# Optimization experiments

Hardware: AMD Instinct MI355X
Metric: run time of the kernel (lower is better)

## Reference

```python
import jax, jax.numpy as jnp
import numpy as np

EPS = 1e-08
MAX_DELTA_LOG = 0.3
N = 1_000_000
DEG = 4
E = N * DEG
H = 64


def setup_inputs() -> dict:
    key = jax.random.key(0)
    k1, k2, k3, k4, k5, k6 = jax.random.split(key, 6)
    hu_scalar = jax.random.normal(k1, (N,), dtype=jnp.float32) * 50.0 + 100.0
    neighbor_indices = jax.random.randint(k2, (E,), 0, N, dtype=jnp.int64)
    neighbor_offsets = (jnp.arange(N + 1, dtype=jnp.int64) * DEG)  # fixed degree-4 CSR
    W_nei1 = jax.random.normal(k3, (1, H), dtype=jnp.float32) * 0.01
    W_self1 = jax.random.normal(k4, (1, H), dtype=jnp.float32) * 0.01
    b1 = jnp.zeros((H,), dtype=jnp.float32)
    W_nei2 = jax.random.normal(k5, (H,), dtype=jnp.float32) * 0.01
    W_self2 = jax.random.normal(k6, (H,), dtype=jnp.float32) * 0.01
    b2 = jnp.zeros((1,), dtype=jnp.float32)
    return {
        'hu_scalar': hu_scalar,
        'neighbor_indices': neighbor_indices,
        'neighbor_offsets': neighbor_offsets,
        'W_nei1': W_nei1,
        'W_self1': W_self1,
        'b1': b1,
        'W_nei2': W_nei2,
        'W_self2': W_self2,
        'b2': b2,
    }


def reference(hu_scalar, neighbor_indices, neighbor_offsets, W_nei1, W_self1, b1, W_nei2, W_self2, b2):
    n = neighbor_offsets.shape[0] - 1
    e = neighbor_indices.shape[0]
    counts = neighbor_offsets[1:] - neighbor_offsets[:-1]
    # CSR row ids for each edge: repeat_interleave(arange(N), counts)
    row_ids = jnp.repeat(jnp.arange(n, dtype=jnp.int64), counts, total_repeat_length=e)

    h = hu_scalar.astype(jnp.float32)
    mu = h.mean()
    sigma = h.std(ddof=1) + EPS  # torch.std is unbiased
    h0 = (h - mu) / sigma  # (N,)

    # layer 1: scatter-sum of scalar neighbor features
    nei_sum0 = jax.ops.segment_sum(h0[neighbor_indices], row_ids, num_segments=n)  # (N,)
    h1 = jax.nn.relu(b1 + nei_sum0[:, None] * W_nei1 + h0[:, None] * W_self1)  # (N, H)

    # layer 2: scatter-sum of (N,H) features
    nei_sum1 = jax.ops.segment_sum(h1[neighbor_indices], row_ids, num_segments=n)  # (N, H)
    delta_raw = b2 + nei_sum1 @ W_nei2 + h1 @ W_self2  # (N,)
    return MAX_DELTA_LOG * jnp.tanh(delta_raw)
```

## Files before the change

kernel.cpp:

```cpp
#include <hip/hip_runtime.h>
#include <math.h>

#define RED_BLOCKS 1024
#define BLK 256
#define HDIM 64

__global__ void k_reduce_partial(const float* __restrict__ hu, int n,
                                 double* __restrict__ part) {
  __shared__ double ls[BLK];
  __shared__ double lq[BLK];
  double s = 0.0, q = 0.0;
  for (int i = blockIdx.x * BLK + threadIdx.x; i < n; i += gridDim.x * BLK) {
    double v = (double)hu[i];
    s += v;
    q += v * v;
  }
  ls[threadIdx.x] = s;
  lq[threadIdx.x] = q;
  __syncthreads();
  for (int off = BLK / 2; off > 0; off >>= 1) {
    if (threadIdx.x < off) {
      ls[threadIdx.x] += ls[threadIdx.x + off];
      lq[threadIdx.x] += lq[threadIdx.x + off];
    }
    __syncthreads();
  }
  if (threadIdx.x == 0) {
    part[blockIdx.x] = ls[0];
    part[RED_BLOCKS + blockIdx.x] = lq[0];
  }
}

__global__ void k_reduce_final(const double* __restrict__ part, int n,
                               float* __restrict__ stats) {
  __shared__ double ls[BLK];
  __shared__ double lq[BLK];
  double s = 0.0, q = 0.0;
  for (int i = threadIdx.x; i < RED_BLOCKS; i += BLK) {
    s += part[i];
    q += part[RED_BLOCKS + i];
  }
  ls[threadIdx.x] = s;
  lq[threadIdx.x] = q;
  __syncthreads();
  for (int off = BLK / 2; off > 0; off >>= 1) {
    if (threadIdx.x < off) {
      ls[threadIdx.x] += ls[threadIdx.x + off];
      lq[threadIdx.x] += lq[threadIdx.x + off];
    }
    __syncthreads();
  }
  if (threadIdx.x == 0) {
    double sum = ls[0], sumsq = lq[0];
    double mu = sum / (double)n;
    double var = (sumsq - sum * sum / (double)n) / (double)(n - 1);
    if (var < 0.0) var = 0.0;
    double sigma = sqrt(var) + 1e-8;
    stats[0] = (float)mu;
    stats[1] = (float)(1.0 / sigma);
  }
}

__global__ void k_layer1(const float* __restrict__ hu,
                         const int* __restrict__ nbr,
                         const float* __restrict__ Wn1,
                         const float* __restrict__ Ws1,
                         const float* __restrict__ B1,
                         const float* __restrict__ Wn2,
                         const float* __restrict__ Ws2,
                         const float* __restrict__ stats,
                         float* __restrict__ snei,
                         float* __restrict__ sself,
                         int n) {
  __shared__ float wn1[HDIM], ws1[HDIM], bb1[HDIM], wn2[HDIM], ws2[HDIM];
  int t = threadIdx.x;
  if (t < HDIM) {
    wn1[t] = Wn1[t];
    ws1[t] = Ws1[t];
    bb1[t] = B1[t];
    wn2[t] = Wn2[t];
    ws2[t] = Ws2[t];
  }
  __syncthreads();
  int u = blockIdx.x * BLK + threadIdx.x;
  if (u >= n) return;
  float mu = stats[0];
  float inv = stats[1];
  int4 nb = ((const int4*)nbr)[u];
  float hsum = hu[nb.x] + hu[nb.y] + hu[nb.z] + hu[nb.w];
  float a = (hsum - 4.0f * mu) * inv;
  float c = (hu[u] - mu) * inv;
  float sn = 0.0f, ss = 0.0f;
#pragma unroll
  for (int j = 0; j < HDIM; ++j) {
    float tt = fmaf(a, wn1[j], fmaf(c, ws1[j], bb1[j]));
    float r = fmaxf(tt, 0.0f);
    sn = fmaf(r, wn2[j], sn);
    ss = fmaf(r, ws2[j], ss);
  }
  snei[u] = sn;
  if (sself != nullptr) sself[u] = ss;
}

__global__ void k_layer2(const int* __restrict__ nbr,
                         const float* __restrict__ snei,
                         const float* __restrict__ sself,
                         const float* __restrict__ B2,
                         float* __restrict__ out,
                         int n) {
  int u = blockIdx.x * BLK + threadIdx.x;
  if (u >= n) return;
  int4 nb = ((const int4*)nbr)[u];
  float s = snei[nb.x] + snei[nb.y] + snei[nb.z] + snei[nb.w];
  float d = B2[0] + s + sself[u];
  out[u] = 0.3f * tanhf(d);
}

__global__ void k_layer2_rc(const float* __restrict__ hu,
                            const int* __restrict__ nbr,
                            const float* __restrict__ Wn1,
                            const float* __restrict__ Ws1,
                            const float* __restrict__ B1,
                            const float* __restrict__ Ws2,
                            const float* __restrict__ stats,
                            const float* __restrict__ snei,
                            const float* __restrict__ B2,
                            float* __restrict__ out,
                            int n) {
  __shared__ float wn1[HDIM], ws1[HDIM], bb1[HDIM], ws2[HDIM];
  int t = threadIdx.x;
  if (t < HDIM) {
    wn1[t] = Wn1[t];
    ws1[t] = Ws1[t];
    bb1[t] = B1[t];
    ws2[t] = Ws2[t];
  }
  __syncthreads();
  int u = blockIdx.x * BLK + threadIdx.x;
  if (u >= n) return;
  float mu = stats[0];
  float inv = stats[1];
  int4 nb = ((const int4*)nbr)[u];
  float hsum = hu[nb.x] + hu[nb.y] + hu[nb.z] + hu[nb.w];
  float a = (hsum - 4.0f * mu) * inv;
  float c = (hu[u] - mu) * inv;
  float ss = 0.0f;
#pragma unroll
  for (int j = 0; j < HDIM; ++j) {
    float tt = fmaf(a, wn1[j], fmaf(c, ws1[j], bb1[j]));
    float r = fmaxf(tt, 0.0f);
    ss = fmaf(r, ws2[j], ss);
  }
  float s = snei[nb.x] + snei[nb.y] + snei[nb.z] + snei[nb.w];
  float d = B2[0] + s + ss;
  out[u] = 0.3f * tanhf(d);
}

extern "C" void kernel_launch(void* const* d_in, const int* in_sizes, int n_in,
                              void* d_out, int out_size, void* d_ws, size_t ws_size,
                              hipStream_t stream) {
  const float* hu  = (const float*)d_in[0];
  const int*   nbr = (const int*)d_in[1];
  const float* Wn1 = (const float*)d_in[3];
  const float* Ws1 = (const float*)d_in[4];
  const float* B1  = (const float*)d_in[5];
  const float* Wn2 = (const float*)d_in[6];
  const float* Ws2 = (const float*)d_in[7];
  const float* B2  = (const float*)d_in[8];
  float* out = (float*)d_out;
  const int n = in_sizes[0];

  char* ws = (char*)d_ws;
  double* part = (double*)ws;
  float* stats = (float*)(ws + 2 * RED_BLOCKS * 8);
  float* snei  = (float*)(ws + 32768);
  size_t need_full = 32768 + 2 * (size_t)n * sizeof(float);
  size_t need_half = 32768 + (size_t)n * sizeof(float);

  k_reduce_partial<<<RED_BLOCKS, BLK, 0, stream>>>(hu, n, part);
  k_reduce_final<<<1, BLK, 0, stream>>>(part, n, stats);

  int blocks = (n + BLK - 1) / BLK;
  if (ws_size >= need_full) {
    float* sself = snei + n;
    k_layer1<<<blocks, BLK, 0, stream>>>(hu, nbr, Wn1, Ws1, B1, Wn2, Ws2, stats,
                                         snei, sself, n);
    k_layer2<<<blocks, BLK, 0, stream>>>(nbr, snei, sself, B2, out, n);
  } else if (ws_size >= need_half) {
    k_layer1<<<blocks, BLK, 0, stream>>>(hu, nbr, Wn1, Ws1, B1, Wn2, Ws2, stats,
                                         snei, nullptr, n);
    k_layer2_rc<<<blocks, BLK, 0, stream>>>(hu, nbr, Wn1, Ws1, B1, Ws2, stats,
                                            snei, B2, out, n);
  }
}
```

Baseline: 63.55 us.

## Vectorize reduction and layer-1 loop, use nontemporal loads/stores, drop fallback path

The stats reduction now reads hu as float4 and handles the tail on one thread. Layer-1's hidden loop works on 4-wide float vectors held in shared memory, and the neighbor index loads and the intermediate and output stores become nontemporal. Launch bounds are added everywhere, and the recompute fallback for a small workspace is removed, so a full-size workspace is now assumed. The aim is fewer memory instructions and less cache pollution from streamed data, at the cost of failing if the workspace is smaller than 2N floats.

```diff
diff --git a/kernel.cpp b/kernel.cpp
--- a/kernel.cpp
+++ b/kernel.cpp
@@ -5,15 +5,28 @@
 #define BLK 256
 #define HDIM 64
 
-__global__ void k_reduce_partial(const float* __restrict__ hu, int n,
-                                 double* __restrict__ part) {
+typedef int   v4i __attribute__((ext_vector_type(4)));
+typedef float v4f __attribute__((ext_vector_type(4)));
+
+__global__ void __launch_bounds__(BLK) k_reduce_partial(const float* __restrict__ hu, int n,
+                                                        double* __restrict__ part) {
   __shared__ double ls[BLK];
   __shared__ double lq[BLK];
+  const v4f* hu4 = (const v4f*)hu;
+  const int n4 = n >> 2;
   double s = 0.0, q = 0.0;
-  for (int i = blockIdx.x * BLK + threadIdx.x; i < n; i += gridDim.x * BLK) {
-    double v = (double)hu[i];
-    s += v;
-    q += v * v;
+  for (int i = blockIdx.x * BLK + threadIdx.x; i < n4; i += RED_BLOCKS * BLK) {
+    v4f v = hu4[i];
+    double a = (double)v.x, b = (double)v.y, c = (double)v.z, d = (double)v.w;
+    s += a + b + c + d;
+    q += a * a + b * b + c * c + d * d;
+  }
+  if (blockIdx.x == 0 && threadIdx.x == 0) {
+    for (int i = n4 << 2; i < n; ++i) {
+      double v = (double)hu[i];
+      s += v;
+      q += v * v;
+    }
   }
   ls[threadIdx.x] = s;
   lq[threadIdx.x] = q;
@@ -31,8 +44,8 @@
   }
 }
 
-__global__ void k_reduce_final(const double* __restrict__ part, int n,
-                               float* __restrict__ stats) {
+__global__ void __launch_bounds__(BLK) k_reduce_final(const double* __restrict__ part, int n,
+                                                      float* __restrict__ stats) {
   __shared__ double ls[BLK];
   __shared__ double lq[BLK];
   double s = 0.0, q = 0.0;
@@ -61,99 +74,67 @@
   }
 }
 
-__global__ void k_layer1(const float* __restrict__ hu,
-                         const int* __restrict__ nbr,
-                         const float* __restrict__ Wn1,
-                         const float* __restrict__ Ws1,
-                         const float* __restrict__ B1,
-                         const float* __restrict__ Wn2,
-                         const float* __restrict__ Ws2,
-                         const float* __restrict__ stats,
-                         float* __restrict__ snei,
-                         float* __restrict__ sself,
-                         int n) {
-  __shared__ float wn1[HDIM], ws1[HDIM], bb1[HDIM], wn2[HDIM], ws2[HDIM];
+__global__ void __launch_bounds__(BLK) k_layer1(
+    const float* __restrict__ hu,
+    const int* __restrict__ nbr,
+    const float* __restrict__ Wn1,
+    const float* __restrict__ Ws1,
+    const float* __restrict__ B1,
+    const float* __restrict__ Wn2,
+    const float* __restrict__ Ws2,
+    const float* __restrict__ stats,
+    float* __restrict__ snei,
+    float* __restrict__ sself,
+    int n) {
+  __shared__ v4f wn1v[HDIM / 4], ws1v[HDIM / 4], bb1v[HDIM / 4], wn2v[HDIM / 4], ws2v[HDIM / 4];
   int t = threadIdx.x;
   if (t < HDIM) {
-    wn1[t] = Wn1[t];
-    ws1[t] = Ws1[t];
-    bb1[t] = B1[t];
-    wn2[t] = Wn2[t];
-    ws2[t] = Ws2[t];
+    ((float*)wn1v)[t] = Wn1[t];
+    ((float*)ws1v)[t] = Ws1[t];
+    ((float*)bb1v)[t] = B1[t];
+    ((float*)wn2v)[t] = Wn2[t];
+    ((float*)ws2v)[t] = Ws2[t];
   }
   __syncthreads();
   int u = blockIdx.x * BLK + threadIdx.x;
   if (u >= n) return;
-  float mu = stats[0];
-  float inv = stats[1];
-  int4 nb = ((const int4*)nbr)[u];
+  const float mu = stats[0];
+  const float inv = stats[1];
+  v4i nb = __builtin_nontemporal_load((const v4i*)nbr + u);
   float hsum = hu[nb.x] + hu[nb.y] + hu[nb.z] + hu[nb.w];
   float a = (hsum - 4.0f * mu) * inv;
   float c = (hu[u] - mu) * inv;
-  float sn = 0.0f, ss = 0.0f;
+  v4f av = {a, a, a, a};
+  v4f cv = {c, c, c, c};
+  v4f z = {0.0f, 0.0f, 0.0f, 0.0f};
+  v4f sn4 = z, ss4 = z;
 #pragma unroll
-  for (int j = 0; j < HDIM; ++j) {
-    float tt = fmaf(a, wn1[j], fmaf(c, ws1[j], bb1[j]));
-    float r = fmaxf(tt, 0.0f);
-    sn = fmaf(r, wn2[j], sn);
-    ss = fmaf(r, ws2[j], ss);
+  for (int j = 0; j < HDIM / 4; ++j) {
+    v4f tt = av * wn1v[j] + cv * ws1v[j] + bb1v[j];
+    v4f r = __builtin_elementwise_max(tt, z);
+    sn4 += r * wn2v[j];
+    ss4 += r * ws2v[j];
   }
-  snei[u] = sn;
-  if (sself != nullptr) sself[u] = ss;
+  float sn = (sn4.x + sn4.y) + (sn4.z + sn4.w);
+  float ss = (ss4.x + ss4.y) + (ss4.z + ss4.w);
+  __builtin_nontemporal_store(sn, snei + u);
+  __builtin_nontemporal_store(ss, sself + u);
 }
 
-__global__ void k_layer2(const int* __restrict__ nbr,
-                         const float* __restrict__ snei,
-                         const float* __restrict__ sself,
-                         const float* __restrict__ B2,
-                         float* __restrict__ out,
-                         int n) {
+__global__ void __launch_bounds__(BLK) k_layer2(
+    const int* __restrict__ nbr,
+    const float* __restrict__ snei,
+    const float* __restrict__ sself,
+    const float* __restrict__ B2,
+    float* __restrict__ out,
+    int n) {
   int u = blockIdx.x * BLK + threadIdx.x;
   if (u >= n) return;
-  int4 nb = ((const int4*)nbr)[u];
+  v4i nb = __builtin_nontemporal_load((const v4i*)nbr + u);
   float s = snei[nb.x] + snei[nb.y] + snei[nb.z] + snei[nb.w];
-  float d = B2[0] + s + sself[u];
-  out[u] = 0.3f * tanhf(d);
-}
-
-__global__ void k_layer2_rc(const float* __restrict__ hu,
-                            const int* __restrict__ nbr,
-                            const float* __restrict__ Wn1,
-                            const float* __restrict__ Ws1,
-                            const float* __restrict__ B1,
-                            const float* __restrict__ Ws2,
-                            const float* __restrict__ stats,
-                            const float* __restrict__ snei,
-                            const float* __restrict__ B2,
-                            float* __restrict__ out,
-                            int n) {
-  __shared__ float wn1[HDIM], ws1[HDIM], bb1[HDIM], ws2[HDIM];
-  int t = threadIdx.x;
-  if (t < HDIM) {
-    wn1[t] = Wn1[t];
-    ws1[t] = Ws1[t];
-    bb1[t] = B1[t];
-    ws2[t] = Ws2[t];
-  }
-  __syncthreads();
-  int u = blockIdx.x * BLK + threadIdx.x;
-  if (u >= n) return;
-  float mu = stats[0];
-  float inv = stats[1];
-  int4 nb = ((const int4*)nbr)[u];
-  float hsum = hu[nb.x] + hu[nb.y] + hu[nb.z] + hu[nb.w];
-  float a = (hsum - 4.0f * mu) * inv;
-  float c = (hu[u] - mu) * inv;
-  float ss = 0.0f;
-#pragma unroll
-  for (int j = 0; j < HDIM; ++j) {
-    float tt = fmaf(a, wn1[j], fmaf(c, ws1[j], bb1[j]));
-    float r = fmaxf(tt, 0.0f);
-    ss = fmaf(r, ws2[j], ss);
-  }
-  float s = snei[nb.x] + snei[nb.y] + snei[nb.z] + snei[nb.w];
+  float ss = __builtin_nontemporal_load(sself + u);
   float d = B2[0] + s + ss;
-  out[u] = 0.3f * tanhf(d);
+  __builtin_nontemporal_store(0.3f * tanhf(d), out + u);
 }
 
 extern "C" void kernel_launch(void* const* d_in, const int* in_sizes, int n_in,
@@ -174,22 +155,13 @@
   double* part = (double*)ws;
   float* stats = (float*)(ws + 2 * RED_BLOCKS * 8);
   float* snei  = (float*)(ws + 32768);
-  size_t need_full = 32768 + 2 * (size_t)n * sizeof(float);
-  size_t need_half = 32768 + (size_t)n * sizeof(float);
+  float* sself = snei + n;
 
   k_reduce_partial<<<RED_BLOCKS, BLK, 0, stream>>>(hu, n, part);
   k_reduce_final<<<1, BLK, 0, stream>>>(part, n, stats);
 
   int blocks = (n + BLK - 1) / BLK;
-  if (ws_size >= need_full) {
-    float* sself = snei + n;
-    k_layer1<<<blocks, BLK, 0, stream>>>(hu, nbr, Wn1, Ws1, B1, Wn2, Ws2, stats,
-                                         snei, sself, n);
-    k_layer2<<<blocks, BLK, 0, stream>>>(nbr, snei, sself, B2, out, n);
-  } else if (ws_size >= need_half) {
-    k_layer1<<<blocks, BLK, 0, stream>>>(hu, nbr, Wn1, Ws1, B1, Wn2, Ws2, stats,
-                                         snei, nullptr, n);
-    k_layer2_rc<<<blocks, BLK, 0, stream>>>(hu, nbr, Wn1, Ws1, B1, Ws2, stats,
-                                            snei, B2, out, n);
-  }
+  k_layer1<<<blocks, BLK, 0, stream>>>(hu, nbr, Wn1, Ws1, B1, Wn2, Ws2, stats,
+                                       snei, sself, n);
+  k_layer2<<<blocks, BLK, 0, stream>>>(nbr, snei, sself, B2, out, n);
 }
```

After: 63.66 us. Within noise of the previous version (+0.2%).
